# Optimization experiments

Measured on AMD Instinct MI355X. Metric: run time of the kernel, lower is better.

The kernel has to match this reference:

```python
import jax, jax.numpy as jnp
import numpy as np

PI = 3.141592653589793


def setup_inputs() -> dict:
    key = jax.random.key(0)
    k1, k2, k3, k4 = jax.random.split(key, 4)
    B, D, Q, L, C = 8192, 4096, 16, 24, 512
    features = jax.random.normal(k1, (B, D), dtype=jnp.float32)
    projection_w = jax.random.normal(k2, (Q, D), dtype=jnp.float32) * (1.0 / np.sqrt(D))
    projection_b = jnp.zeros((Q,), dtype=jnp.float32)
    vqc_weights = jax.random.uniform(k3, (L, Q, 3), dtype=jnp.float32, minval=0.0, maxval=2.0 * PI)
    linear_w = jax.random.normal(k4, (Q, C), dtype=jnp.float32) * 0.1
    linear_b = jnp.zeros((C,), dtype=jnp.float32)
    return {
        "features": features,
        "projection_w": projection_w,
        "projection_b": projection_b,
        "vqc_weights": vqc_weights,
        "linear_w": linear_w,
        "linear_b": linear_b,
    }


def _vqc_forward(angles, vqc_weights):
    # angles: (B, Q) data-encoding RY angles; vqc_weights: (L, Q, 3)
    # Per-qubit Bloch-vector simulation (no entanglement).
    # Start |0> -> Bloch (0,0,1); RY(a) gives (sin a, 0, cos a).
    x = jnp.sin(angles)
    y = jnp.zeros_like(angles)
    z = jnp.cos(angles)

    def layer(carry, w):
        x, y, z = carry
        phi, theta, omega = w[:, 0], w[:, 1], w[:, 2]  # each (Q,), broadcast over B
        # RZ(phi): rotate about Z
        cp, sp = jnp.cos(phi), jnp.sin(phi)
        x1 = x * cp - y * sp
        y1 = x * sp + y * cp
        # RY(theta): rotate about Y
        ct, st = jnp.cos(theta), jnp.sin(theta)
        x2 = x1 * ct + z * st
        z2 = -x1 * st + z * ct
        # RZ(omega)
        co, so = jnp.cos(omega), jnp.sin(omega)
        x3 = x2 * co - y1 * so
        y3 = x2 * so + y1 * co
        return (x3, y3, z2), None

    (x, y, z), _ = jax.lax.scan(layer, (x, y, z), vqc_weights)
    return z  # <Z> expectation per qubit, (B, Q)


def reference(features, projection_w, projection_b, vqc_weights, linear_w, linear_b):
    # classical projection to per-qubit angles, squashed to (-pi, pi)
    proj = features @ projection_w.T + projection_b  # (B, Q)
    angles = PI * jnp.tanh(proj)
    qubits = _vqc_forward(angles, vqc_weights)  # (B, Q)
    return qubits @ linear_w + linear_b  # (B, C)
```

## Files before the change

### kernel.cpp

```cpp
#include <hip/hip_runtime.h>
#include <hip/hip_bf16.h>

using short8  = __attribute__((ext_vector_type(8))) short;
using floatx4 = __attribute__((ext_vector_type(4))) float;

constexpr int D  = 4096;
constexpr int Q  = 16;
constexpr int L  = 24;
constexpr int C  = 512;
constexpr int RB = 16;
constexpr int NW = 8;
constexpr int KW = D / NW;
constexpr int NSTEP = KW / 32;
constexpr float PI_F = 3.14159265358979323846f;

__device__ inline void cvt8(const float4& v0, const float4& v1,
                            short8& hi, short8& lo) {
    const float f[8] = {v0.x, v0.y, v0.z, v0.w, v1.x, v1.y, v1.z, v1.w};
    #pragma unroll
    for (int j = 0; j < 8; ++j) {
        union { float f; unsigned u; } a, b, c;
        a.f = f[j];
        hi[j] = (short)(a.u >> 16);
        b.u = a.u & 0xFFFF0000u;
        c.f = a.f - b.f;
        lo[j] = (short)(c.u >> 16);
    }
}

__global__ __launch_bounds__(512, 4)
void vqc_fused(const float* __restrict__ feat,
               const float* __restrict__ pw,
               const float* __restrict__ pb,
               const float* __restrict__ vw,
               const float* __restrict__ lw,
               const float* __restrict__ lb,
               float* __restrict__ out, int B)
{
    __shared__ float s_red[NW][RB][Q];
    __shared__ float s_trig[L * Q * 6];
    __shared__ float s_qub[RB][Q];

    const int t    = threadIdx.x;
    const int wave = t >> 6;
    const int lane = t & 63;
    const int row0 = blockIdx.x * RB;
    const int mrow = lane & 15;
    const int quad = lane >> 4;

    if (t < L * Q) {
        const float phi = vw[t * 3 + 0], th = vw[t * 3 + 1], om = vw[t * 3 + 2];
        float* tr = s_trig + t * 6;
        tr[0] = cosf(phi); tr[1] = sinf(phi);
        tr[2] = cosf(th);  tr[3] = sinf(th);
        tr[4] = cosf(om);  tr[5] = sinf(om);
    }

    int rr = row0 + mrow; if (rr >= B) rr = B - 1;
    const float* ap = feat + (size_t)rr * D + wave * KW + quad * 8;
    const float* bp = pw   + (size_t)mrow * D + wave * KW + quad * 8;

    floatx4 acc = {0.f, 0.f, 0.f, 0.f};
    #pragma unroll 4
    for (int s = 0; s < NSTEP; ++s) {
        const float4 a0 = *(const float4*)(ap + s * 32);
        const float4 a1 = *(const float4*)(ap + s * 32 + 4);
        const float4 b0 = *(const float4*)(bp + s * 32);
        const float4 b1 = *(const float4*)(bp + s * 32 + 4);
        short8 ah, al, bh, bl;
        cvt8(a0, a1, ah, al);
        cvt8(b0, b1, bh, bl);
        acc = __builtin_amdgcn_mfma_f32_16x16x32_bf16(al, bh, acc, 0, 0, 0);
        acc = __builtin_amdgcn_mfma_f32_16x16x32_bf16(ah, bl, acc, 0, 0, 0);
        acc = __builtin_amdgcn_mfma_f32_16x16x32_bf16(ah, bh, acc, 0, 0, 0);
    }
    #pragma unroll
    for (int i = 0; i < 4; ++i)
        s_red[wave][quad * 4 + i][mrow] = acc[i];
    __syncthreads();

    if (t < RB * Q) {
        const int r = t >> 4, q = t & 15;
        float p = 0.f;
        #pragma unroll
        for (int w = 0; w < NW; ++w) p += s_red[w][r][q];
        p += pb[q];
        const float angle = PI_F * tanhf(p);
        float x = sinf(angle), y = 0.f, z = cosf(angle);
        #pragma unroll
        for (int l = 0; l < L; ++l) {
            const float* w6 = s_trig + (l * 16 + q) * 6;
            const float cp = w6[0], sp = w6[1];
            const float ct = w6[2], st = w6[3];
            const float co = w6[4], so = w6[5];
            const float x1 = x * cp - y * sp;
            const float y1 = x * sp + y * cp;
            const float x2 = x1 * ct + z * st;
            const float z2 = -x1 * st + z * ct;
            x = x2 * co - y1 * so;
            y = x2 * so + y1 * co;
            z = z2;
        }
        s_qub[r][q] = z;
    }
    __syncthreads();

    {
        const int c = t;
        float wv[Q];
        #pragma unroll
        for (int q = 0; q < Q; ++q) wv[q] = lw[(size_t)q * C + c];
        const float lbv = lb[c];
        #pragma unroll 4
        for (int r = 0; r < RB; ++r) {
            if (row0 + r >= B) break;
            float a2 = lbv;
            #pragma unroll
            for (int q = 0; q < Q; ++q) a2 = fmaf(s_qub[r][q], wv[q], a2);
            out[(size_t)(row0 + r) * C + c] = a2;
        }
    }
}

extern "C" void kernel_launch(void* const* d_in, const int* in_sizes, int n_in,
                              void* d_out, int out_size, void* d_ws, size_t ws_size,
                              hipStream_t stream) {
    const float *feat = nullptr, *pw = nullptr, *pb = nullptr,
                *vw = nullptr, *lw = nullptr, *lb = nullptr;
    long long B = 0;
    bool ok = false;
    if (n_in == 6) {
        int imax = 0;
        for (int i = 1; i < 6; ++i)
            if ((long long)in_sizes[i] > (long long)in_sizes[imax]) imax = i;
        const long long scales[2] = {1, 4};
        for (int s = 0; s < 2 && !ok; ++s) {
            const long long sc = scales[s];
            int m[6] = {imax, -1, -1, -1, -1, -1};
            bool good = ((long long)in_sizes[imax] % (sc * D)) == 0;
            for (int i = 0; i < 6 && good; ++i) {
                if (i == imax) continue;
                long long e = (long long)in_sizes[i];
                if (e % sc) { good = false; break; }
                e /= sc;
                if      (e == 65536 && m[1] < 0) m[1] = i;
                else if (e == 16    && m[2] < 0) m[2] = i;
                else if (e == 1152  && m[3] < 0) m[3] = i;
                else if (e == 8192  && m[4] < 0) m[4] = i;
                else if (e == 512   && m[5] < 0) m[5] = i;
                else good = false;
            }
            if (good && m[1] >= 0 && m[2] >= 0 && m[3] >= 0 && m[4] >= 0 && m[5] >= 0) {
                feat = (const float*)d_in[m[0]];
                pw   = (const float*)d_in[m[1]];
                pb   = (const float*)d_in[m[2]];
                vw   = (const float*)d_in[m[3]];
                lw   = (const float*)d_in[m[4]];
                lb   = (const float*)d_in[m[5]];
                B = (long long)in_sizes[imax] / (sc * D);
                ok = true;
            }
        }
    }
    if (!ok) {
        feat = (const float*)d_in[0];
        pw   = (const float*)d_in[1];
        pb   = (const float*)d_in[2];
        vw   = (const float*)d_in[3];
        lw   = (const float*)d_in[4];
        lb   = (const float*)d_in[5];
        B = in_sizes[0] / D;
    }
    float* out = (float*)d_out;

    const int nblocks = (int)((B + RB - 1) / RB);
    dim3 grid(nblocks), block(512);
    hipLaunchKernelGGL(vqc_fused, grid, block, 0, stream,
                       feat, pw, pb, vw, lw, lb, out, (int)B);
}
```

Baseline: 205.7 us.

## Stage projection GEMM tiles through LDS with async global_load_lds double buffering

Replaces the per-wave direct global loads of features and projection weights with a chunked loop that stages 256-wide K slices of both into LDS using global_load_lds DMA. Two buffers are used so the next chunk loads while the current one is consumed, and rows are XOR-swizzled to avoid bank conflicts. The aim is to overlap the feature stream with the MFMA work and hide load latency. In exchange it adds 64KB of LDS per block, which limits occupancy, and a barrier on every chunk. The trig table setup now runs after the GEMM instead of overlapping with it.

```diff
diff --git a/kernel.cpp b/kernel.cpp
--- a/kernel.cpp
+++ b/kernel.cpp
@@ -1,17 +1,16 @@
 #include <hip/hip_runtime.h>
-#include <hip/hip_bf16.h>
 
 using short8  = __attribute__((ext_vector_type(8))) short;
 using floatx4 = __attribute__((ext_vector_type(4))) float;
 
-constexpr int D  = 4096;
-constexpr int Q  = 16;
-constexpr int L  = 24;
-constexpr int C  = 512;
-constexpr int RB = 16;
-constexpr int NW = 8;
-constexpr int KW = D / NW;
-constexpr int NSTEP = KW / 32;
+constexpr int D   = 4096;
+constexpr int Q   = 16;
+constexpr int L   = 24;
+constexpr int C   = 512;
+constexpr int RB  = 16;
+constexpr int NW  = 8;
+constexpr int BK  = 256;
+constexpr int NCH = D / BK;
 constexpr float PI_F = 3.14159265358979323846f;
 
 __device__ inline void cvt8(const float4& v0, const float4& v1,
@@ -28,6 +27,12 @@
     }
 }
 
+__device__ inline void gll16(const void* g, void* l) {
+    __builtin_amdgcn_global_load_lds(
+        (const __attribute__((address_space(1))) void*)g,
+        (__attribute__((address_space(3))) void*)l, 16, 0, 0);
+}
+
 __global__ __launch_bounds__(512, 4)
 void vqc_fused(const float* __restrict__ feat,
                const float* __restrict__ pw,
@@ -37,9 +42,7 @@
                const float* __restrict__ lb,
                float* __restrict__ out, int B)
 {
-    __shared__ float s_red[NW][RB][Q];
-    __shared__ float s_trig[L * Q * 6];
-    __shared__ float s_qub[RB][Q];
+    __shared__ __align__(16) float lds[16384];
 
     const int t    = threadIdx.x;
     const int wave = t >> 6;
@@ -48,6 +51,52 @@
     const int mrow = lane & 15;
     const int quad = lane >> 4;
 
+    const int r_a = wave * 2;
+
+    floatx4 acc = {0.f, 0.f, 0.f, 0.f};
+
+    auto stage = [&](int c, int b) {
+        #pragma unroll
+        for (int i = 0; i < 2; ++i) {
+            const int r   = r_a + i;
+            const int off = (lane * 16) ^ ((r & 7) << 4);
+            int rr = row0 + r; if (rr >= B) rr = B - 1;
+            const char* ga = (const char*)(feat + (size_t)rr * D + (size_t)c * BK) + off;
+            const char* gb = (const char*)(pw   + (size_t)r  * D + (size_t)c * BK) + off;
+            gll16(ga, (void*)&lds[(size_t)b * 4096 + r * BK]);
+            gll16(gb, (void*)&lds[8192 + (size_t)b * 4096 + r * BK]);
+        }
+    };
+
+    stage(0, 0);
+
+    const int sw = (mrow & 7) << 4;
+    const int cb = (wave * 32 + quad * 8) * 4;
+    for (int c = 0; c < NCH; ++c) {
+        __syncthreads();
+        if (c + 1 < NCH) stage(c + 1, (c + 1) & 1);
+
+        const char* arow = (const char*)&lds[(size_t)(c & 1) * 4096 + mrow * BK];
+        const char* brow = (const char*)&lds[8192 + (size_t)(c & 1) * 4096 + mrow * BK];
+        const float4 a0 = *(const float4*)(arow + ((cb     ) ^ sw));
+        const float4 a1 = *(const float4*)(arow + ((cb + 16) ^ sw));
+        const float4 b0 = *(const float4*)(brow + ((cb     ) ^ sw));
+        const float4 b1 = *(const float4*)(brow + ((cb + 16) ^ sw));
+        short8 ah, al, bh, bl;
+        cvt8(a0, a1, ah, al);
+        cvt8(b0, b1, bh, bl);
+        acc = __builtin_amdgcn_mfma_f32_16x16x32_bf16(al, bh, acc, 0, 0, 0);
+        acc = __builtin_amdgcn_mfma_f32_16x16x32_bf16(ah, bl, acc, 0, 0, 0);
+        acc = __builtin_amdgcn_mfma_f32_16x16x32_bf16(ah, bh, acc, 0, 0, 0);
+    }
+
+    float* s_red = lds;
+    #pragma unroll
+    for (int i = 0; i < 4; ++i)
+        s_red[(wave * RB + quad * 4 + i) * Q + mrow] = acc[i];
+    __syncthreads();
+
+    float* s_trig = lds + 2048;
     if (t < L * Q) {
         const float phi = vw[t * 3 + 0], th = vw[t * 3 + 1], om = vw[t * 3 + 2];
         float* tr = s_trig + t * 6;
@@ -55,35 +104,14 @@
         tr[2] = cosf(th);  tr[3] = sinf(th);
         tr[4] = cosf(om);  tr[5] = sinf(om);
     }
-
-    int rr = row0 + mrow; if (rr >= B) rr = B - 1;
-    const float* ap = feat + (size_t)rr * D + wave * KW + quad * 8;
-    const float* bp = pw   + (size_t)mrow * D + wave * KW + quad * 8;
-
-    floatx4 acc = {0.f, 0.f, 0.f, 0.f};
-    #pragma unroll 4
-    for (int s = 0; s < NSTEP; ++s) {
-        const float4 a0 = *(const float4*)(ap + s * 32);
-        const float4 a1 = *(const float4*)(ap + s * 32 + 4);
-        const float4 b0 = *(const float4*)(bp + s * 32);
-        const float4 b1 = *(const float4*)(bp + s * 32 + 4);
-        short8 ah, al, bh, bl;
-        cvt8(a0, a1, ah, al);
-        cvt8(b0, b1, bh, bl);
-        acc = __builtin_amdgcn_mfma_f32_16x16x32_bf16(al, bh, acc, 0, 0, 0);
-        acc = __builtin_amdgcn_mfma_f32_16x16x32_bf16(ah, bl, acc, 0, 0, 0);
-        acc = __builtin_amdgcn_mfma_f32_16x16x32_bf16(ah, bh, acc, 0, 0, 0);
-    }
-    #pragma unroll
-    for (int i = 0; i < 4; ++i)
-        s_red[wave][quad * 4 + i][mrow] = acc[i];
     __syncthreads();
 
+    float* s_qub = lds + 2048 + L * Q * 6;
     if (t < RB * Q) {
         const int r = t >> 4, q = t & 15;
         float p = 0.f;
         #pragma unroll
-        for (int w = 0; w < NW; ++w) p += s_red[w][r][q];
+        for (int w = 0; w < NW; ++w) p += s_red[(w * RB + r) * Q + q];
         p += pb[q];
         const float angle = PI_F * tanhf(p);
         float x = sinf(angle), y = 0.f, z = cosf(angle);
@@ -101,23 +129,23 @@
             y = x2 * so + y1 * co;
             z = z2;
         }
-        s_qub[r][q] = z;
+        s_qub[r * Q + q] = z;
     }
     __syncthreads();
 
     {
-        const int c = t;
+        const int cidx = t;
         float wv[Q];
         #pragma unroll
-        for (int q = 0; q < Q; ++q) wv[q] = lw[(size_t)q * C + c];
-        const float lbv = lb[c];
+        for (int q = 0; q < Q; ++q) wv[q] = lw[(size_t)q * C + cidx];
+        const float lbv = lb[cidx];
         #pragma unroll 4
         for (int r = 0; r < RB; ++r) {
             if (row0 + r >= B) break;
             float a2 = lbv;
             #pragma unroll
-            for (int q = 0; q < Q; ++q) a2 = fmaf(s_qub[r][q], wv[q], a2);
-            out[(size_t)(row0 + r) * C + c] = a2;
+            for (int q = 0; q < Q; ++q) a2 = fmaf(s_qub[r * Q + q], wv[q], a2);
+            out[(size_t)(row0 + r) * C + cidx] = a2;
         }
     }
 }
```

Result: no change. 206.0 us (+0.1%).
